# Kernel optimization log

Hardware: AMD Instinct MI355X
Metric: run time of the kernel (lower is better)

Reference implementation:

```python
import jax, jax.numpy as jnp
import numpy as np

N, E, H = 4096, 32768, 4
NUM_GRAPHS = 8
NEG_SLOPE_ATT = 0.2   # GATConv internal leaky_relu
NEG_SLOPE_ACT = 0.01  # F.leaky_relu default


def _glorot(k, shape):
    lim = (6.0 / (shape[0] + shape[-1])) ** 0.5
    return jax.random.uniform(k, shape, jnp.float32, -lim, lim)


def setup_inputs() -> dict:
    key = jax.random.key(0)
    ks = jax.random.split(key, 24)
    d = {}
    d["x_graph"] = jax.random.normal(ks[0], (N, 256), jnp.float32)
    d["action"] = jax.random.normal(ks[1], (N, 128), jnp.float32)
    d["temp_img"] = jax.random.normal(ks[2], (N, 128), jnp.float32)
    d["edge_attr"] = jax.random.normal(ks[3], (E, 16), jnp.float32)
    d["edge_index"] = jax.random.randint(ks[4], (2, E), 0, N)
    d["batch"] = jnp.sort(jax.random.randint(ks[5], (N,), 0, NUM_GRAPHS))
    # conv1: GATConv(512 -> 512, heads=4, edge_dim=16)
    d["W1"] = _glorot(ks[6], (512, H * 512))
    d["att_src1"] = _glorot(ks[7], (H, 512))
    d["att_dst1"] = _glorot(ks[8], (H, 512))
    d["att_edge1"] = _glorot(ks[9], (H, 512))
    d["We1"] = _glorot(ks[10], (16, H * 512))
    d["b1"] = jnp.zeros((H * 512,), jnp.float32)
    # conv2: GATConv(2048 -> 2048, heads=4, edge_dim=16)
    d["W2"] = _glorot(ks[11], (2048, H * 2048))
    d["att_src2"] = _glorot(ks[12], (H, 2048))
    d["att_dst2"] = _glorot(ks[13], (H, 2048))
    d["att_edge2"] = _glorot(ks[14], (H, 2048))
    d["We2"] = _glorot(ks[15], (16, H * 2048))
    d["b2"] = jnp.zeros((H * 2048,), jnp.float32)
    # fc_output: Linear(512*heads*heads=8192 -> 256)
    d["Wout"] = _glorot(ks[16], (8192, 256))
    d["bout"] = jnp.zeros((256,), jnp.float32)
    return d


def _gat(x, src, dst, eattr, W, a_s, a_d, a_e, We, b, C):
    # PyG GATConv: shared lin for src/dst, edge features in attention, softmax per dst.
    h = (x @ W).reshape(N, H, C)             # [N,H,C]
    ea = (eattr @ We).reshape(-1, H, C)      # [Ef,H,C]
    e = (h * a_s).sum(-1)[src] + (h * a_d).sum(-1)[dst] + (ea * a_e).sum(-1)  # [Ef,H]
    e = jax.nn.leaky_relu(e, NEG_SLOPE_ATT)
    m = jax.ops.segment_max(e, dst, num_segments=N)      # self-loops ensure every dst occupied
    ex = jnp.exp(e - m[dst])
    s = jax.ops.segment_sum(ex, dst, num_segments=N)
    alpha = ex / s[dst]                                   # [Ef,H]
    out = jax.ops.segment_sum(alpha[:, :, None] * h[src], dst, num_segments=N)  # [N,H,C]
    return out.reshape(N, H * C) + b


def _forward(x_graph, action, temp_img, edge_attr,
             W1, att_src1, att_dst1, att_edge1, We1, b1,
             W2, att_src2, att_dst2, att_edge2, We2, b2,
             Wout, bout, edge_index, batch):
    x = jnp.concatenate([x_graph, action, temp_img], axis=1)  # [N,512]
    src, dst = edge_index[0], edge_index[1]
    # add self-loops with fill_value='mean' for edge_attr (mean of incoming edge attrs)
    deg = jax.ops.segment_sum(jnp.ones((E,), x.dtype), dst, num_segments=N)
    loop_attr = jax.ops.segment_sum(edge_attr, dst, num_segments=N) / jnp.maximum(deg, 1.0)[:, None]
    loop = jnp.arange(N)
    src_f = jnp.concatenate([src, loop])
    dst_f = jnp.concatenate([dst, loop])
    ea_f = jnp.concatenate([edge_attr, loop_attr], axis=0)
    x = jax.nn.leaky_relu(_gat(x, src_f, dst_f, ea_f, W1, att_src1, att_dst1, att_edge1, We1, b1, 512), NEG_SLOPE_ACT)
    x = jax.nn.leaky_relu(_gat(x, src_f, dst_f, ea_f, W2, att_src2, att_dst2, att_edge2, We2, b2, 2048), NEG_SLOPE_ACT)
    x = jax.nn.leaky_relu(x @ Wout + bout, NEG_SLOPE_ACT)     # [N,256]
    sums = jax.ops.segment_sum(x, batch, num_segments=NUM_GRAPHS)
    cnt = jax.ops.segment_sum(jnp.ones((N,), x.dtype), batch, num_segments=NUM_GRAPHS)
    return sums / jnp.maximum(cnt, 1.0)[:, None]              # [NUM_GRAPHS,256]


def reference(x_graph, action, temp_img, edge_attr,
              W1, att_src1, att_dst1, att_edge1, We1, b1,
              W2, att_src2, att_dst2, att_edge2, We2, b2,
              Wout, bout, edge_index, batch):
    return _forward(x_graph, action, temp_img, edge_attr,
                    W1, att_src1, att_dst1, att_edge1, We1, b1,
                    W2, att_src2, att_dst2, att_edge2, We2, b2,
                    Wout, bout, edge_index, batch)
```

## Files before the change

kernel.cpp:

```cpp
#include <hip/hip_runtime.h>
#include <math.h>

constexpr int Nn  = 4096;
constexpr int Ne  = 32768;
constexpr int NEf = Ne + Nn;

constexpr size_t OFF_X    = 0;
constexpr size_t OFF_WT1H = 0;
constexpr size_t OFF_WT1L = 524288;
constexpr size_t OFF_Z1HI = 2097152;
constexpr size_t OFF_Z1LO = 6291456;
constexpr size_t OFF_X2HI = 2097152;
constexpr size_t OFF_X2LO = 6291456;
constexpr size_t OFF_PART = 2097152;
constexpr size_t OFF_X2   = 10485760;
constexpr size_t OFF_X3   = 10485760;
constexpr size_t OFF_H    = 18874368;
constexpr size_t OFF_WOH  = 25165824;
constexpr size_t OFF_WOL  = 26214400;
constexpr size_t OFF_YP   = 27262976;
constexpr size_t OFF_LP  = 31457280;
constexpr size_t OFF_WS1 = OFF_LP  + 65536;
constexpr size_t OFF_WD1 = OFF_WS1 + 2048;
constexpr size_t OFF_WS2 = OFF_WD1 + 2048;
constexpr size_t OFF_WD2 = OFF_WS2 + 8192;
constexpr size_t OFF_AE1 = OFF_WD2 + 8192;
constexpr size_t OFF_AE2 = OFF_AE1 + 64;
constexpr size_t OFF_AS1 = OFF_AE2 + 64;
constexpr size_t OFF_AD1 = OFF_AS1 + 16384;
constexpr size_t OFF_AS2 = OFF_AD1 + 16384;
constexpr size_t OFF_AD2 = OFF_AS2 + 16384;
constexpr size_t OFF_EB  = OFF_AD2 + 16384;
constexpr size_t OFF_AL  = OFF_EB  + (size_t)NEf*4;
constexpr size_t OFF_I   = OFF_AL  + (size_t)NEf*4;
constexpr size_t I_DEG = 0;
constexpr size_t I_RP  = 4096;
constexpr size_t I_CUR = 8200;
constexpr size_t I_EID = 12296;
constexpr size_t WS_FLOATS = OFF_I + I_EID + (size_t)NEf + 64;

using bf16x8 = __bf16 __attribute__((ext_vector_type(8)));
using f16x8  = _Float16 __attribute__((ext_vector_type(8)));
using f32x4  = float __attribute__((ext_vector_type(4)));

__device__ __forceinline__ float wred64(float v){
#pragma unroll
  for (int o = 32; o > 0; o >>= 1) v += __shfl_down(v, o, 64);
  return v;
}
__device__ __forceinline__ float lrelu(float v, float s){ return v > 0.f ? v : s * v; }

__device__ __forceinline__ unsigned short f2bf(float x){
  unsigned int u = __float_as_uint(x);
  unsigned int r = (u + 0x7FFFu + ((u >> 16) & 1u)) >> 16;
  return (unsigned short)r;
}
__device__ __forceinline__ float bf2f(unsigned short h){
  return __uint_as_float((unsigned int)h << 16);
}
__device__ __forceinline__ void split2(float x, unsigned short& h, unsigned short& l){
  h = f2bf(x);
  l = f2bf(x - bf2f(h));
}
__device__ __forceinline__ unsigned short f2h(float x){
  _Float16 h = (_Float16)x;
  return __builtin_bit_cast(unsigned short, h);
}
__device__ __forceinline__ float h2f(unsigned short u){
  return (float)__builtin_bit_cast(_Float16, u);
}
__device__ __forceinline__ void split2h(float x, unsigned short& h, unsigned short& l){
  _Float16 hh = (_Float16)x;
  h = __builtin_bit_cast(unsigned short, hh);
  _Float16 ll = (_Float16)(x - (float)hh);
  l = __builtin_bit_cast(unsigned short, ll);
}
__device__ __forceinline__ void gload16(const void* g, void* l){
  __builtin_amdgcn_global_load_lds((const __attribute__((address_space(1))) void*)g,
                                   (__attribute__((address_space(3))) void*)l, 16, 0, 0);
}

__global__ void k_concat(const float* __restrict__ xg, const float* __restrict__ ac,
                         const float* __restrict__ ti, float* __restrict__ x){
  int i = blockIdx.x * 256 + threadIdx.x;
  int n = i >> 9, c = i & 511;
  float v;
  if (c < 256)      v = xg[(size_t)n*256 + c];
  else if (c < 384) v = ac[(size_t)n*128 + (c-256)];
  else              v = ti[(size_t)n*128 + (c-384)];
  x[i] = v;
}

__global__ void k_count(const int* __restrict__ ei, int* __restrict__ deg){
  int e = blockIdx.x * 256 + threadIdx.x;
  if (e < Ne) atomicAdd(&deg[ei[Ne + e]], 1);
}

__global__ void k_scan(const int* __restrict__ deg, int* __restrict__ rowptr, int* __restrict__ cursor){
  __shared__ int sd[1024];
  int t = threadIdx.x;
  int v[4]; int s = 0;
#pragma unroll
  for (int i = 0; i < 4; i++){ v[i] = s; s += deg[t*4 + i] + 1; }
  sd[t] = s;
  __syncthreads();
  for (int off = 1; off < 1024; off <<= 1){
    int x = (t >= off) ? sd[t - off] : 0;
    __syncthreads();
    sd[t] += x;
    __syncthreads();
  }
  int base = (t == 0) ? 0 : sd[t - 1];
#pragma unroll
  for (int i = 0; i < 4; i++){ int rp = base + v[i]; rowptr[t*4 + i] = rp; cursor[t*4 + i] = rp; }
  if (t == 1023) rowptr[4096] = sd[1023];
}

__global__ void k_fill(const int* __restrict__ ei, int* __restrict__ cursor, int* __restrict__ eids){
  int e = blockIdx.x * 256 + threadIdx.x;
  if (e >= NEf) return;
  int d = (e < Ne) ? ei[Ne + e] : (e - Ne);
  int p = atomicAdd(&cursor[d], 1);
  eids[p] = e;
}

__global__ void k_sort(const int* __restrict__ rowptr, int* __restrict__ eids){
  int n = blockIdx.x * 256 + threadIdx.x;
  if (n >= Nn) return;
  int b = rowptr[n], e = rowptr[n + 1];
  for (int i = b + 1; i < e; i++){
    int key = eids[i]; int j = i - 1;
    while (j >= b && eids[j] > key){ eids[j+1] = eids[j]; j--; }
    eids[j+1] = key;
  }
}

__global__ void k_loopattr(const float* __restrict__ eattr, const int* __restrict__ rowptr,
                           const int* __restrict__ eids, float* __restrict__ lp){
  int idx = blockIdx.x * 256 + threadIdx.x;
  int n = idx >> 4, a = idx & 15;
  if (n >= Nn) return;
  int b = rowptr[n], e = rowptr[n + 1];
  float s = 0.f; int cnt = 0;
  for (int j = b; j < e; ++j){
    int id = eids[j];
    if (id < Ne){ s += eattr[(size_t)id*16 + a]; cnt++; }
  }
  lp[(size_t)n*16 + a] = s / fmaxf((float)cnt, 1.f);
}

__global__ void k_proj(const float* __restrict__ W, const float* __restrict__ a_s,
                       const float* __restrict__ a_d, float* __restrict__ Ws,
                       float* __restrict__ Wd, int K, int C){
  int gid = blockIdx.x * 256 + threadIdx.x;
  int wave = gid >> 6, lane = gid & 63;
  int h = wave & 3, k = wave >> 2;
  if (k >= K) return;
  const float* wrow = W + (size_t)k * (4*C) + (size_t)h * C;
  const float* ar = a_s + (size_t)h * C;
  const float* dr = a_d + (size_t)h * C;
  float ps = 0.f, pd = 0.f;
  for (int c = lane; c < C; c += 64){ float w = wrow[c]; ps += w * ar[c]; pd += w * dr[c]; }
  ps = wred64(ps); pd = wred64(pd);
  if (lane == 0){ Ws[k*4 + h] = ps; Wd[k*4 + h] = pd; }
}

__global__ void k_aeproj(const float* __restrict__ We, const float* __restrict__ ae,
                         float* __restrict__ outp, int C){
  int gid = blockIdx.x * 256 + threadIdx.x;
  int wave = gid >> 6, lane = gid & 63;
  int h = wave & 3, k = wave >> 2;
  if (k >= 16) return;
  const float* wrow = We + (size_t)k * (4*C) + (size_t)h * C;
  const float* ar = ae + (size_t)h * C;
  float s = 0.f;
  for (int c = lane; c < C; c += 64) s += wrow[c] * ar[c];
  s = wred64(s);
  if (lane == 0) outp[k*4 + h] = s;
}

__global__ __launch_bounds__(256) void k_asad(const float* __restrict__ x, const float* __restrict__ Ws,
                      const float* __restrict__ Wd, float* __restrict__ as_,
                      float* __restrict__ ad_, int D){
  int n = blockIdx.x, t = threadIdx.x;
  const float* row = x + (size_t)n * D;
  float p[8] = {0,0,0,0,0,0,0,0};
  for (int c = t; c < D; c += 256){
    float xv = row[c];
    float4 ws4 = *(const float4*)&Ws[c*4];
    float4 wd4 = *(const float4*)&Wd[c*4];
    p[0] += xv * ws4.x; p[1] += xv * ws4.y; p[2] += xv * ws4.z; p[3] += xv * ws4.w;
    p[4] += xv * wd4.x; p[5] += xv * wd4.y; p[6] += xv * wd4.z; p[7] += xv * wd4.w;
  }
  __shared__ float sm[4][8];
  int lane = t & 63, wid = t >> 6;
#pragma unroll
  for (int q = 0; q < 8; q++){
    float v = wred64(p[q]);
    if (lane == 0) sm[wid][q] = v;
  }
  __syncthreads();
  if (t < 8){
    float s = sm[0][t] + sm[1][t] + sm[2][t] + sm[3][t];
    if (t < 4) as_[(size_t)n*4 + t] = s;
    else       ad_[(size_t)n*4 + (t-4)] = s;
  }
}

__global__ void k_edge(const float* __restrict__ eattr, const float* __restrict__ lp,
                       const int* __restrict__ ei, const float* __restrict__ as_,
                       const float* __restrict__ ad_, const float* __restrict__ aep,
                       float* __restrict__ ebuf){
  int e = blockIdx.x * 256 + threadIdx.x;
  if (e >= NEf) return;
  int s, d; const float* ea;
  if (e < Ne){ s = ei[e]; d = ei[Ne + e]; ea = eattr + (size_t)e * 16; }
  else { s = e - Ne; d = e - Ne; ea = lp + (size_t)(e - Ne) * 16; }
  float eav[16];
#pragma unroll
  for (int k = 0; k < 16; k++) eav[k] = ea[k];
#pragma unroll
  for (int h = 0; h < 4; h++){
    float v = as_[(size_t)s*4 + h] + ad_[(size_t)d*4 + h];
#pragma unroll
    for (int k = 0; k < 16; k++) v += eav[k] * aep[k*4 + h];
    ebuf[(size_t)e*4 + h] = lrelu(v, 0.2f);
  }
}

__global__ __launch_bounds__(256) void k_softmax(const int* __restrict__ rowptr, const int* __restrict__ eids,
                          const float* __restrict__ ebuf, float* __restrict__ alpha){
  const int wid = threadIdx.x >> 6, lane = threadIdx.x & 63;
  const int n = blockIdx.x * 4 + wid;
  const int b = rowptr[n], e = rowptr[n + 1];
  float4 m = {-1e30f, -1e30f, -1e30f, -1e30f};
  for (int j = b + lane; j < e; j += 64){
    float4 ev = *(const float4*)&ebuf[(size_t)eids[j]*4];
    m.x = fmaxf(m.x, ev.x); m.y = fmaxf(m.y, ev.y);
    m.z = fmaxf(m.z, ev.z); m.w = fmaxf(m.w, ev.w);
  }
#pragma unroll
  for (int o = 32; o > 0; o >>= 1){
    m.x = fmaxf(m.x, __shfl_xor(m.x, o, 64));
    m.y = fmaxf(m.y, __shfl_xor(m.y, o, 64));
    m.z = fmaxf(m.z, __shfl_xor(m.z, o, 64));
    m.w = fmaxf(m.w, __shfl_xor(m.w, o, 64));
  }
  float4 s = {0.f, 0.f, 0.f, 0.f};
  for (int j = b + lane; j < e; j += 64){
    int eid = eids[j];
    float4 ev = *(const float4*)&ebuf[(size_t)eid*4];
    float4 ex = { expf(ev.x - m.x), expf(ev.y - m.y), expf(ev.z - m.z), expf(ev.w - m.w) };
    *(float4*)&alpha[(size_t)eid*4] = ex;
    s.x += ex.x; s.y += ex.y; s.z += ex.z; s.w += ex.w;
  }
#pragma unroll
  for (int o = 32; o > 0; o >>= 1){
    s.x += __shfl_xor(s.x, o, 64);
    s.y += __shfl_xor(s.y, o, 64);
    s.z += __shfl_xor(s.z, o, 64);
    s.w += __shfl_xor(s.w, o, 64);
  }
  float4 r = { 1.f/s.x, 1.f/s.y, 1.f/s.z, 1.f/s.w };
  for (int j = b + lane; j < e; j += 64){
    int eid = eids[j];
    float4 av = *(const float4*)&alpha[(size_t)eid*4];
    av.x *= r.x; av.y *= r.y; av.z *= r.z; av.w *= r.w;
    *(float4*)&alpha[(size_t)eid*4] = av;
  }
}

__global__ __launch_bounds__(256) void k_agg1_split(const float* __restrict__ x, const float* __restrict__ alpha,
                      const int* __restrict__ rowptr, const int* __restrict__ eids,
                      const int* __restrict__ ei, unsigned short* __restrict__ z1hi,
                      unsigned short* __restrict__ z1lo){
  int n = blockIdx.x, t = threadIdx.x;
  float2 a0 = {0,0}, a1 = {0,0}, a2 = {0,0}, a3 = {0,0};
  int b = rowptr[n], e = rowptr[n + 1];
  for (int j = b; j < e; ++j){
    int eid = eids[j];
    int s = (eid < Ne) ? ei[eid] : (eid - Ne);
    float4 av = *(const float4*)&alpha[(size_t)eid*4];
    float2 xv = *(const float2*)&x[(size_t)s*512 + t*2];
    a0.x += av.x*xv.x; a0.y += av.x*xv.y;
    a1.x += av.y*xv.x; a1.y += av.y*xv.y;
    a2.x += av.z*xv.x; a2.y += av.z*xv.y;
    a3.x += av.w*xv.x; a3.y += av.w*xv.y;
  }
  size_t base = (size_t)n*2048 + t*2;
  float2 av[4] = {a0, a1, a2, a3};
#pragma unroll
  for (int h = 0; h < 4; h++){
    ushort2 hh, ll;
    split2(av[h].x, hh.x, ll.x);
    split2(av[h].y, hh.y, ll.y);
    *(ushort2*)&z1hi[base + h*512] = hh;
    *(ushort2*)&z1lo[base + h*512] = ll;
  }
}

__global__ void k_splitx2(const float* __restrict__ x2, unsigned short* __restrict__ xh,
                          unsigned short* __restrict__ xl){
  int i = blockIdx.x * 256 + threadIdx.x;
  float4 v = ((const float4*)x2)[i];
  ushort4 h, l;
  split2h(v.x, h.x, l.x); split2h(v.y, h.y, l.y);
  split2h(v.z, h.z, l.z); split2h(v.w, h.w, l.w);
  ((ushort4*)xh)[i] = h;
  ((ushort4*)xl)[i] = l;
}

__global__ __launch_bounds__(256) void k_agg2b(const unsigned short* __restrict__ H,
                      const float* __restrict__ alpha,
                      const int* __restrict__ rowptr, const int* __restrict__ eids,
                      const int* __restrict__ ei, unsigned short* __restrict__ x3,
                      const float* __restrict__ b2, int h){
  int n = blockIdx.x, t = threadIdx.x;
  float acc[8] = {0,0,0,0,0,0,0,0};
  int b = rowptr[n], e = rowptr[n + 1];
  for (int j = b; j < e; ++j){
    int eid = eids[j];
    int s = (eid < Ne) ? ei[eid] : (eid - Ne);
    float a = alpha[(size_t)eid*4 + h];
    f16x8 hv = *(const f16x8*)&H[(size_t)s*2048 + t*8];
#pragma unroll
    for (int q = 0; q < 8; q++) acc[q] += a * (float)hv[q];
  }
  const float* bb = b2 + (size_t)h*2048 + t*8;
  ushort4 o0, o1;
  float4 b0 = *(const float4*)bb;
  float4 b1 = *(const float4*)(bb + 4);
  o0.x = f2h(lrelu(acc[0] + b0.x, 0.01f)); o0.y = f2h(lrelu(acc[1] + b0.y, 0.01f));
  o0.z = f2h(lrelu(acc[2] + b0.z, 0.01f)); o0.w = f2h(lrelu(acc[3] + b0.w, 0.01f));
  o1.x = f2h(lrelu(acc[4] + b1.x, 0.01f)); o1.y = f2h(lrelu(acc[5] + b1.y, 0.01f));
  o1.z = f2h(lrelu(acc[6] + b1.z, 0.01f)); o1.w = f2h(lrelu(acc[7] + b1.w, 0.01f));
  size_t base = (size_t)n*2048 + t*8;
  *(ushort4*)&x3[base]     = o0;
  *(ushort4*)&x3[base + 4] = o1;
}

template<bool HALF, bool STORELO>
__global__ __launch_bounds__(256) void k_wsplit(const float* __restrict__ W, int ldw, int coloff, int K,
                       unsigned short* __restrict__ whi, unsigned short* __restrict__ wlo){
  __shared__ float tile[32][33];
  int bk = blockIdx.x * 32, bn = blockIdx.y * 32;
  int tx = threadIdx.x & 31, ty = threadIdx.x >> 5;
#pragma unroll
  for (int i = 0; i < 4; i++){
    int k = bk + ty + i*8;
    tile[ty + i*8][tx] = W[(size_t)k*ldw + coloff + bn + tx];
  }
  __syncthreads();
#pragma unroll
  for (int i = 0; i < 4; i++){
    int n = bn + ty + i*8;
    float v = tile[tx][ty + i*8];
    unsigned short hh, ll;
    if (HALF) split2h(v, hh, ll); else split2(v, hh, ll);
    whi[(size_t)n*K + bk + tx] = hh;
    if (STORELO) wlo[(size_t)n*K + bk + tx] = ll;
  }
}

__global__ __launch_bounds__(512) void k_gemm256(
    const unsigned short* __restrict__ Ah, const unsigned short* __restrict__ Al,
    const unsigned short* __restrict__ Bh, unsigned short* __restrict__ Cout)
{
  __shared__ __align__(16) unsigned short lds[49152];
  const int t = threadIdx.x;
  const int bid = blockIdx.y * 8 + blockIdx.x;
  const int sbid = (bid & 7) * 32 + (bid >> 3);
  const int brow = (sbid >> 3) * 128, bcol = (sbid & 7) * 256;
  const int w = t >> 6, lane = t & 63;
  const int wm = (w >> 2) * 64, wn = (w & 3) * 64;
  constexpr int BUF = 16384, BOFF = 8192;

  const int asr = t >> 3;
  const int ascc = (t & 7) ^ (asr & 7);
  const unsigned short* asrc = (ascc < 4 ? Ah : Al) + (size_t)(brow + asr)*2048 + (size_t)(ascc & 3)*8;
  const int bsr = t >> 2;
  const int bscc = (t & 3) ^ ((bsr >> 1) & 3);
  const unsigned short* bsrc = Bh + (size_t)(bcol + bsr)*2048 + (size_t)bscc*8;
  const int adst = w * 512;
  const int bdst = BOFF + w * 512;

  const int fr = lane & 15, kc = lane >> 4;
  const int aswz = (kc ^ (lane & 7)) * 8;
  const int bswz = (kc ^ ((lane >> 1) & 3)) * 8;
  int aoff[4], boff[4];
#pragma unroll
  for (int m = 0; m < 4; m++) aoff[m] = (wm + m*16 + fr)*64 + aswz;
#pragma unroll
  for (int n = 0; n < 4; n++) boff[n] = BOFF + (wn + n*16 + fr)*32 + bswz;

  f32x4 acc[4][4];
#pragma unroll
  for (int m = 0; m < 4; m++)
#pragma unroll
    for (int n = 0; n < 4; n++) acc[m][n] = f32x4{0.f, 0.f, 0.f, 0.f};

  gload16(asrc,                        &lds[adst]);
  gload16(asrc + (size_t)64*2048,      &lds[4096 + adst]);
  gload16(bsrc,                        &lds[bdst]);
  gload16(bsrc + (size_t)128*2048,     &lds[4096 + bdst]);
  gload16(asrc + 32,                   &lds[BUF + adst]);
  gload16(asrc + (size_t)64*2048 + 32, &lds[BUF + 4096 + adst]);
  gload16(bsrc + 32,                   &lds[BUF + bdst]);
  gload16(bsrc + (size_t)128*2048 + 32,&lds[BUF + 4096 + bdst]);
  asm volatile("s_waitcnt vmcnt(4)" ::: "memory");
  __builtin_amdgcn_s_barrier();

  for (int kt = 0; kt < 64; ++kt){
    const int bufo = (kt % 3) * BUF;
    const int nbo  = ((kt + 2) % 3) * BUF;
    const size_t nko = (size_t)(kt + 2) * 32;
    const bool pf = (kt + 2) < 64;

    f16x8 ah[4], al[4];
#pragma unroll
    for (int m = 0; m < 4; m++){
      ah[m] = *(const f16x8*)&lds[bufo + aoff[m]];
      al[m] = *(const f16x8*)&lds[bufo + (aoff[m] ^ 32)];
    }
    {
      f16x8 b0 = *(const f16x8*)&lds[bufo + boff[0]];
      f16x8 b1 = *(const f16x8*)&lds[bufo + boff[1]];
      if (pf){
        gload16(asrc + nko,                   &lds[nbo + adst]);
        gload16(asrc + (size_t)64*2048 + nko, &lds[nbo + 4096 + adst]);
      }
      __builtin_amdgcn_s_barrier();
      asm volatile("s_waitcnt lgkmcnt(0)");
      __builtin_amdgcn_s_setprio(1);
#pragma unroll
      for (int m = 0; m < 4; m++) acc[m][0] = __builtin_amdgcn_mfma_f32_16x16x32_f16(ah[m], b0, acc[m][0], 0, 0, 0);
#pragma unroll
      for (int m = 0; m < 4; m++) acc[m][0] = __builtin_amdgcn_mfma_f32_16x16x32_f16(al[m], b0, acc[m][0], 0, 0, 0);
#pragma unroll
      for (int m = 0; m < 4; m++) acc[m][1] = __builtin_amdgcn_mfma_f32_16x16x32_f16(ah[m], b1, acc[m][1], 0, 0, 0);
#pragma unroll
      for (int m = 0; m < 4; m++) acc[m][1] = __builtin_amdgcn_mfma_f32_16x16x32_f16(al[m], b1, acc[m][1], 0, 0, 0);
      __builtin_amdgcn_s_setprio(0);
      __builtin_amdgcn_s_barrier();
    }
    {
      f16x8 b2 = *(const f16x8*)&lds[bufo + boff[2]];
      f16x8 b3 = *(const f16x8*)&lds[bufo + boff[3]];
      if (pf){
        gload16(bsrc + nko,                    &lds[nbo + bdst]);
        gload16(bsrc + (size_t)128*2048 + nko, &lds[nbo + 4096 + bdst]);
      }
      __builtin_amdgcn_s_barrier();
      asm volatile("s_waitcnt lgkmcnt(0)");
      __builtin_amdgcn_s_setprio(1);
#pragma unroll
      for (int m = 0; m < 4; m++) acc[m][2] = __builtin_amdgcn_mfma_f32_16x16x32_f16(ah[m], b2, acc[m][2], 0, 0, 0);
#pragma unroll
      for (int m = 0; m < 4; m++) acc[m][2] = __builtin_amdgcn_mfma_f32_16x16x32_f16(al[m], b2, acc[m][2], 0, 0, 0);
#pragma unroll
      for (int m = 0; m < 4; m++) acc[m][3] = __builtin_amdgcn_mfma_f32_16x16x32_f16(ah[m], b3, acc[m][3], 0, 0, 0);
#pragma unroll
      for (int m = 0; m < 4; m++) acc[m][3] = __builtin_amdgcn_mfma_f32_16x16x32_f16(al[m], b3, acc[m][3], 0, 0, 0);
      __builtin_amdgcn_s_setprio(0);
      __builtin_amdgcn_s_barrier();
    }
    if (pf) asm volatile("s_waitcnt vmcnt(4)" ::: "memory");
    else    asm volatile("s_waitcnt vmcnt(0)" ::: "memory");
    __builtin_amdgcn_s_barrier();
  }

#pragma unroll
  for (int m = 0; m < 4; m++){
    const int row0 = brow + wm + m*16 + kc*4;
#pragma unroll
    for (int n = 0; n < 4; n++){
      const int col = bcol + wn + n*16 + fr;
#pragma unroll
      for (int r = 0; r < 4; r++)
        Cout[(size_t)(row0 + r)*2048 + col] = f2h(acc[m][n][r]);
    }
  }
}

template<int KLEN, bool EXACTA, bool HALF, bool OUTF32, bool BETA1, bool ACT, bool HASBIAS>
__global__ __launch_bounds__(256) void k_gemm2(
    const unsigned short* __restrict__ Ah, const unsigned short* __restrict__ Al, int lda, size_t az,
    const unsigned short* __restrict__ Bh, const unsigned short* __restrict__ Bl, int ldb, size_t bz,
    void* __restrict__ Cout, int ldc, size_t cz,
    const float* __restrict__ bias, size_t biasz)
{
  __shared__ unsigned short lds[16384];
  const int t = threadIdx.x;
  const int z = blockIdx.z;
  const int brow = blockIdx.y * 128, bcol = blockIdx.x * 128;
  const int wid = t >> 6, lane = t & 63;
  const int wm = (wid >> 1) * 64, wn = (wid & 1) * 64;

  const int sr = t >> 3, sc = t & 7;
  const int scc = sc ^ (sr & 7);
  const unsigned short* asrc = (scc < 4 ? Ah : Al) + (size_t)(brow + sr)*lda + (size_t)z*az + (size_t)(scc & 3)*8;
  const unsigned short* bsrc = (scc < 4 ? Bh : Bl) + (size_t)(bcol + sr)*ldb + (size_t)z*bz + (size_t)(scc & 3)*8;
  unsigned short* adst = &lds[(size_t)wid * 512];
  unsigned short* bdst = &lds[8192 + (size_t)wid * 512];

  const int fr = lane & 15, kc = lane >> 4;
  const int swz = ((kc ^ (lane & 7)) << 3);
  int aoff[4], boff[4];
#pragma unroll
  for (int m = 0; m < 4; m++) aoff[m] = (wm + m*16 + fr)*64 + swz;
#pragma unroll
  for (int n = 0; n < 4; n++) boff[n] = 8192 + (wn + n*16 + fr)*64 + swz;

  f32x4 acc[4][4];
#pragma unroll
  for (int m = 0; m < 4; m++)
#pragma unroll
    for (int n = 0; n < 4; n++) acc[m][n] = f32x4{0.f, 0.f, 0.f, 0.f};

  for (int kt = 0; kt < KLEN/32; ++kt){
    const size_t ko = (size_t)kt * 32;
#pragma unroll
    for (int i = 0; i < 4; i++){
      gload16(asrc + (size_t)i*32*lda + ko, adst + i*2048);
      gload16(bsrc + (size_t)i*32*ldb + ko, bdst + i*2048);
    }
    __syncthreads();

    if (HALF){
      f16x8 ah[4], bh[4], bl[4];
#pragma unroll
      for (int m = 0; m < 4; m++) ah[m] = *(const f16x8*)&lds[aoff[m]];
#pragma unroll
      for (int n = 0; n < 4; n++){
        bh[n] = *(const f16x8*)&lds[boff[n]];
        bl[n] = *(const f16x8*)&lds[boff[n] ^ 32];
      }
#pragma unroll
      for (int m = 0; m < 4; m++)
#pragma unroll
        for (int n = 0; n < 4; n++){
          acc[m][n] = __builtin_amdgcn_mfma_f32_16x16x32_f16(ah[m], bh[n], acc[m][n], 0, 0, 0);
          acc[m][n] = __builtin_amdgcn_mfma_f32_16x16x32_f16(ah[m], bl[n], acc[m][n], 0, 0, 0);
        }
    } else {
      bf16x8 ah[4], al[4], bh[4], bl[4];
#pragma unroll
      for (int m = 0; m < 4; m++){
        ah[m] = *(const bf16x8*)&lds[aoff[m]];
        if (!EXACTA) al[m] = *(const bf16x8*)&lds[aoff[m] ^ 32];
      }
#pragma unroll
      for (int n = 0; n < 4; n++){
        bh[n] = *(const bf16x8*)&lds[boff[n]];
        bl[n] = *(const bf16x8*)&lds[boff[n] ^ 32];
      }
#pragma unroll
      for (int m = 0; m < 4; m++)
#pragma unroll
        for (int n = 0; n < 4; n++){
          acc[m][n] = __builtin_amdgcn_mfma_f32_16x16x32_bf16(ah[m], bh[n], acc[m][n], 0, 0, 0);
          acc[m][n] = __builtin_amdgcn_mfma_f32_16x16x32_bf16(ah[m], bl[n], acc[m][n], 0, 0, 0);
          if (!EXACTA)
            acc[m][n] = __builtin_amdgcn_mfma_f32_16x16x32_bf16(al[m], bh[n], acc[m][n], 0, 0, 0);
        }
    }
    __syncthreads();
  }

  float bv[4] = {0.f, 0.f, 0.f, 0.f};
  if (HASBIAS){
#pragma unroll
    for (int n = 0; n < 4; n++) bv[n] = bias[(size_t)z*biasz + bcol + wn + n*16 + fr];
  }
  float* Cf = (float*)Cout + (size_t)z*cz;
  unsigned short* Cb = (unsigned short*)Cout + (size_t)z*cz;
#pragma unroll
  for (int m = 0; m < 4; m++){
    const int row0 = brow + wm + m*16 + kc*4;
#pragma unroll
    for (int n = 0; n < 4; n++){
      const int col = bcol + wn + n*16 + fr;
#pragma unroll
      for (int r = 0; r < 4; r++){
        float v = acc[m][n][r] + bv[n];
        if (ACT) v = lrelu(v, 0.01f);
        if (OUTF32){
          float* cp = &Cf[(size_t)(row0 + r)*ldc + col];
          if (BETA1) v += *cp;
          *cp = v;
        } else {
          Cb[(size_t)(row0 + r)*ldc + col] = f2bf(v);
        }
      }
    }
  }
}

__global__ void k_gsum(const float* __restrict__ yp, const float* __restrict__ bout,
                       const int* __restrict__ batch, float* __restrict__ part){
  const int s = blockIdx.x, g = blockIdx.y, t = threadIdx.x;
  __shared__ int sb[2];
  if (t < 2){
    int key = g + t, lo = 0, hi = Nn;
    while (lo < hi){ int mid = (lo + hi) >> 1; if (batch[mid] < key) lo = mid + 1; else hi = mid; }
    sb[t] = lo;
  }
  __syncthreads();
  const int b = sb[0], e = sb[1];
  const size_t P = (size_t)Nn * 256;
  float acc = 0.f;
  float bt = bout[t];
  for (int n = b + s; n < e; n += 32){
    size_t i = (size_t)n*256 + t;
    float v = yp[i] + yp[P + i] + yp[2*P + i] + yp[3*P + i] + bt;
    acc += lrelu(v, 0.01f);
  }
  part[(size_t)(g*32 + s)*256 + t] = acc;
}

__global__ void k_gfin(const float* __restrict__ part, const int* __restrict__ batch,
                       float* __restrict__ out){
  const int g = blockIdx.x, t = threadIdx.x;
  __shared__ int sb[2];
  if (t < 2){
    int key = g + t, lo = 0, hi = Nn;
    while (lo < hi){ int mid = (lo + hi) >> 1; if (batch[mid] < key) lo = mid + 1; else hi = mid; }
    sb[t] = lo;
  }
  __syncthreads();
  const int cnt = sb[1] - sb[0];
  float s = 0.f;
#pragma unroll
  for (int k = 0; k < 32; k++) s += part[(size_t)(g*32 + k)*256 + t];
  out[g*256 + t] = s / fmaxf((float)cnt, 1.f);
}

extern "C" void kernel_launch(void* const* d_in, const int* in_sizes, int n_in,
                              void* d_out, int out_size, void* d_ws, size_t ws_size,
                              hipStream_t stream){
  const float* xg    = (const float*)d_in[0];
  const float* ac    = (const float*)d_in[1];
  const float* ti    = (const float*)d_in[2];
  const float* eattr = (const float*)d_in[3];
  const int*   ei    = (const int*)  d_in[4];
  const int*   batch = (const int*)  d_in[5];
  const float* W1    = (const float*)d_in[6];
  const float* as1w  = (const float*)d_in[7];
  const float* ad1w  = (const float*)d_in[8];
  const float* ae1w  = (const float*)d_in[9];
  const float* We1   = (const float*)d_in[10];
  const float* b1    = (const float*)d_in[11];
  const float* W2    = (const float*)d_in[12];
  const float* as2w  = (const float*)d_in[13];
  const float* ad2w  = (const float*)d_in[14];
  const float* ae2w  = (const float*)d_in[15];
  const float* We2   = (const float*)d_in[16];
  const float* b2    = (const float*)d_in[17];
  const float* Wout  = (const float*)d_in[18];
  const float* bout  = (const float*)d_in[19];
  float* out = (float*)d_out;
  float* ws  = (float*)d_ws;
  if (ws_size < WS_FLOATS * sizeof(float)) return;
  int* iws = (int*)(ws + OFF_I);

  unsigned short* z1hi = (unsigned short*)(ws + OFF_Z1HI);
  unsigned short* z1lo = (unsigned short*)(ws + OFF_Z1LO);
  unsigned short* wt1h = (unsigned short*)(ws + OFF_WT1H);
  unsigned short* wt1l = (unsigned short*)(ws + OFF_WT1L);
  unsigned short* x2hi = (unsigned short*)(ws + OFF_X2HI);
  unsigned short* x2lo = (unsigned short*)(ws + OFF_X2LO);
  unsigned short* whi  = (unsigned short*)(ws + OFF_X);
  unsigned short* woh  = (unsigned short*)(ws + OFF_WOH);
  unsigned short* wol  = (unsigned short*)(ws + OFF_WOL);
  unsigned short* Hb   = (unsigned short*)(ws + OFF_H);
  unsigned short* x3   = (unsigned short*)(ws + OFF_X3);

  hipMemsetAsync(iws + I_DEG, 0, Nn * sizeof(int), stream);
  k_concat <<<8192, 256, 0, stream>>>(xg, ac, ti, ws + OFF_X);
  k_count  <<<128,  256, 0, stream>>>(ei, iws + I_DEG);
  k_scan   <<<1,   1024, 0, stream>>>(iws + I_DEG, iws + I_RP, iws + I_CUR);
  k_fill   <<<144,  256, 0, stream>>>(ei, iws + I_CUR, iws + I_EID);
  k_sort   <<<16,   256, 0, stream>>>(iws + I_RP, iws + I_EID);
  k_loopattr<<<256, 256, 0, stream>>>(eattr, iws + I_RP, iws + I_EID, ws + OFF_LP);

  k_proj   <<<512,  256, 0, stream>>>(W1, as1w, ad1w, ws + OFF_WS1, ws + OFF_WD1, 512, 512);
  k_proj   <<<2048, 256, 0, stream>>>(W2, as2w, ad2w, ws + OFF_WS2, ws + OFF_WD2, 2048, 2048);
  k_aeproj <<<16,   256, 0, stream>>>(We1, ae1w, ws + OFF_AE1, 512);
  k_aeproj <<<16,   256, 0, stream>>>(We2, ae2w, ws + OFF_AE2, 2048);
  k_wsplit<true, true><<<dim3(256, 8), 256, 0, stream>>>(Wout, 256, 0, 8192, woh, wol);

  k_asad      <<<4096, 256, 0, stream>>>(ws + OFF_X, ws + OFF_WS1, ws + OFF_WD1, ws + OFF_AS1, ws + OFF_AD1, 512);
  k_edge      <<<144,  256, 0, stream>>>(eattr, ws + OFF_LP, ei, ws + OFF_AS1, ws + OFF_AD1, ws + OFF_AE1, ws + OFF_EB);
  k_softmax   <<<1024, 256, 0, stream>>>(iws + I_RP, iws + I_EID, ws + OFF_EB, ws + OFF_AL);
  k_agg1_split<<<4096, 256, 0, stream>>>(ws + OFF_X, ws + OFF_AL, iws + I_RP, iws + I_EID, ei, z1hi, z1lo);
  k_wsplit<false, true><<<dim3(16, 64), 256, 0, stream>>>(W1, 2048, 0, 512, wt1h, wt1l);
  k_gemm2<512, false, false, true, false, true, true><<<dim3(4, 32, 4), 256, 0, stream>>>(
      z1hi, z1lo, 2048, 512,  wt1h, wt1l, 512, 512*512,
      ws + OFF_X2, 2048, 512,  b1, 512);

  k_asad   <<<4096, 256, 0, stream>>>(ws + OFF_X2, ws + OFF_WS2, ws + OFF_WD2, ws + OFF_AS2, ws + OFF_AD2, 2048);
  k_edge   <<<144,  256, 0, stream>>>(eattr, ws + OFF_LP, ei, ws + OFF_AS2, ws + OFF_AD2, ws + OFF_AE2, ws + OFF_EB);
  k_softmax<<<1024, 256, 0, stream>>>(iws + I_RP, iws + I_EID, ws + OFF_EB, ws + OFF_AL);

  k_splitx2<<<8192, 256, 0, stream>>>(ws + OFF_X2, x2hi, x2lo);

  for (int h = 0; h < 4; ++h){
    k_wsplit<true, false><<<dim3(64, 64), 256, 0, stream>>>(W2, 8192, h*2048, 2048, whi, nullptr);
    k_gemm256 <<<dim3(8, 32), 512, 0, stream>>>(x2hi, x2lo, whi, Hb);
    k_agg2b   <<<4096, 256, 0, stream>>>(Hb, ws + OFF_AL, iws + I_RP, iws + I_EID, ei, x3, b2, h);
    if (h == 0)
      k_gemm2<512, true, true, true, false, false, false><<<dim3(2, 32, 4), 256, 0, stream>>>(
          x3, x3, 2048, 512,  woh + (size_t)h*2048, wol + (size_t)h*2048, 8192, 512,
          ws + OFF_YP, 256, (size_t)Nn*256,  nullptr, 0);
    else
      k_gemm2<512, true, true, true, true, false, false><<<dim3(2, 32, 4), 256, 0, stream>>>(
          x3, x3, 2048, 512,  woh + (size_t)h*2048, wol + (size_t)h*2048, 8192, 512,
          ws + OFF_YP, 256, (size_t)Nn*256,  nullptr, 0);
  }

  k_gsum<<<dim3(32, 8), 256, 0, stream>>>(ws + OFF_YP, bout, batch, ws + OFF_PART);
  k_gfin<<<8, 256, 0, stream>>>(ws + OFF_PART, batch, out);
}
```

Before: 735.5 us.

## Shrink gemm256 block tile to 128x128 with four waves and simpler pipeline

Changes the split-precision fp16 MFMA GEMM from a 128x256 tile with 8 waves to a 128x128 tile with 4 waves. This doubles the grid to 512 blocks and cuts LDS use so more blocks fit per CU. The main loop is also simplified: the two half-steps with their intra-iteration barriers are merged into one MFMA phase, and all prefetch loads are issued up front. The aim is better occupancy and less barrier overhead, at the cost of more global traffic per output from the smaller tile.

```diff
diff --git a/kernel.cpp b/kernel.cpp
--- a/kernel.cpp
+++ b/kernel.cpp
@@ -362,18 +362,18 @@
   }
 }
 
-__global__ __launch_bounds__(512) void k_gemm256(
+__global__ __launch_bounds__(256) void k_gemm256(
     const unsigned short* __restrict__ Ah, const unsigned short* __restrict__ Al,
     const unsigned short* __restrict__ Bh, unsigned short* __restrict__ Cout)
 {
-  __shared__ __align__(16) unsigned short lds[49152];
+  __shared__ __align__(16) unsigned short lds[36864];
   const int t = threadIdx.x;
-  const int bid = blockIdx.y * 8 + blockIdx.x;
-  const int sbid = (bid & 7) * 32 + (bid >> 3);
-  const int brow = (sbid >> 3) * 128, bcol = (sbid & 7) * 256;
+  const int bid = blockIdx.y * 16 + blockIdx.x;
+  const int sbid = (bid & 7) * 64 + (bid >> 3);
+  const int brow = (sbid >> 4) * 128, bcol = (sbid & 15) * 128;
   const int w = t >> 6, lane = t & 63;
-  const int wm = (w >> 2) * 64, wn = (w & 3) * 64;
-  constexpr int BUF = 16384, BOFF = 8192;
+  const int wm = (w >> 1) * 64, wn = (w & 1) * 64;
+  constexpr int BUF = 12288, BOFF = 8192;
 
   const int asr = t >> 3;
   const int ascc = (t & 7) ^ (asr & 7);
@@ -399,15 +399,16 @@
 #pragma unroll
     for (int n = 0; n < 4; n++) acc[m][n] = f32x4{0.f, 0.f, 0.f, 0.f};
 
-  gload16(asrc,                        &lds[adst]);
-  gload16(asrc + (size_t)64*2048,      &lds[4096 + adst]);
-  gload16(bsrc,                        &lds[bdst]);
-  gload16(bsrc + (size_t)128*2048,     &lds[4096 + bdst]);
-  gload16(asrc + 32,                   &lds[BUF + adst]);
-  gload16(asrc + (size_t)64*2048 + 32, &lds[BUF + 4096 + adst]);
-  gload16(bsrc + 32,                   &lds[BUF + bdst]);
-  gload16(bsrc + (size_t)128*2048 + 32,&lds[BUF + 4096 + bdst]);
-  asm volatile("s_waitcnt vmcnt(4)" ::: "memory");
+#pragma unroll
+  for (int tile = 0; tile < 2; tile++){
+    const int bb = tile * BUF;
+    const size_t ko = (size_t)tile * 32;
+#pragma unroll
+    for (int i = 0; i < 4; i++) gload16(asrc + (size_t)i*32*2048 + ko, &lds[bb + i*2048 + adst]);
+#pragma unroll
+    for (int i = 0; i < 2; i++) gload16(bsrc + (size_t)i*64*2048 + ko, &lds[bb + i*2048 + bdst]);
+  }
+  asm volatile("s_waitcnt vmcnt(6)" ::: "memory");
   __builtin_amdgcn_s_barrier();
 
   for (int kt = 0; kt < 64; ++kt){
@@ -416,55 +417,33 @@
     const size_t nko = (size_t)(kt + 2) * 32;
     const bool pf = (kt + 2) < 64;
 
-    f16x8 ah[4], al[4];
+    f16x8 ah[4], al[4], bfr[4];
 #pragma unroll
     for (int m = 0; m < 4; m++){
       ah[m] = *(const f16x8*)&lds[bufo + aoff[m]];
       al[m] = *(const f16x8*)&lds[bufo + (aoff[m] ^ 32)];
     }
-    {
-      f16x8 b0 = *(const f16x8*)&lds[bufo + boff[0]];
-      f16x8 b1 = *(const f16x8*)&lds[bufo + boff[1]];
-      if (pf){
-        gload16(asrc + nko,                   &lds[nbo + adst]);
-        gload16(asrc + (size_t)64*2048 + nko, &lds[nbo + 4096 + adst]);
-      }
-      __builtin_amdgcn_s_barrier();
-      asm volatile("s_waitcnt lgkmcnt(0)");
-      __builtin_amdgcn_s_setprio(1);
-#pragma unroll
-      for (int m = 0; m < 4; m++) acc[m][0] = __builtin_amdgcn_mfma_f32_16x16x32_f16(ah[m], b0, acc[m][0], 0, 0, 0);
-#pragma unroll
-      for (int m = 0; m < 4; m++) acc[m][0] = __builtin_amdgcn_mfma_f32_16x16x32_f16(al[m], b0, acc[m][0], 0, 0, 0);
-#pragma unroll
-      for (int m = 0; m < 4; m++) acc[m][1] = __builtin_amdgcn_mfma_f32_16x16x32_f16(ah[m], b1, acc[m][1], 0, 0, 0);
-#pragma unroll
-      for (int m = 0; m < 4; m++) acc[m][1] = __builtin_amdgcn_mfma_f32_16x16x32_f16(al[m], b1, acc[m][1], 0, 0, 0);
-      __builtin_amdgcn_s_setprio(0);
-      __builtin_amdgcn_s_barrier();
+#pragma unroll
+    for (int n = 0; n < 4; n++) bfr[n] = *(const f16x8*)&lds[bufo + boff[n]];
+
+    if (pf){
+#pragma unroll
+      for (int i = 0; i < 4; i++) gload16(asrc + (size_t)i*32*2048 + nko, &lds[nbo + i*2048 + adst]);
+#pragma unroll
+      for (int i = 0; i < 2; i++) gload16(bsrc + (size_t)i*64*2048 + nko, &lds[nbo + i*2048 + bdst]);
     }
-    {
-      f16x8 b2 = *(const f16x8*)&lds[bufo + boff[2]];
-      f16x8 b3 = *(const f16x8*)&lds[bufo + boff[3]];
-      if (pf){
-        gload16(bsrc + nko,                    &lds[nbo + bdst]);
-        gload16(bsrc + (size_t)128*2048 + nko, &lds[nbo + 4096 + bdst]);
-      }
-      __builtin_amdgcn_s_barrier();
-      asm volatile("s_waitcnt lgkmcnt(0)");
-      __builtin_amdgcn_s_setprio(1);
-#pragma unroll
-      for (int m = 0; m < 4; m++) acc[m][2] = __builtin_amdgcn_mfma_f32_16x16x32_f16(ah[m], b2, acc[m][2], 0, 0, 0);
-#pragma unroll
-      for (int m = 0; m < 4; m++) acc[m][2] = __builtin_amdgcn_mfma_f32_16x16x32_f16(al[m], b2, acc[m][2], 0, 0, 0);
-#pragma unroll
-      for (int m = 0; m < 4; m++) acc[m][3] = __builtin_amdgcn_mfma_f32_16x16x32_f16(ah[m], b3, acc[m][3], 0, 0, 0);
-#pragma unroll
-      for (int m = 0; m < 4; m++) acc[m][3] = __builtin_amdgcn_mfma_f32_16x16x32_f16(al[m], b3, acc[m][3], 0, 0, 0);
-      __builtin_amdgcn_s_setprio(0);
-      __builtin_amdgcn_s_barrier();
+
+    __builtin_amdgcn_s_setprio(1);
+#pragma unroll
+    for (int n = 0; n < 4; n++){
+#pragma unroll
+      for (int m = 0; m < 4; m++) acc[m][n] = __builtin_amdgcn_mfma_f32_16x16x32_f16(ah[m], bfr[n], acc[m][n], 0, 0, 0);
+#pragma unroll
+      for (int m = 0; m < 4; m++) acc[m][n] = __builtin_amdgcn_mfma_f32_16x16x32_f16(al[m], bfr[n], acc[m][n], 0, 0, 0);
     }
-    if (pf) asm volatile("s_waitcnt vmcnt(4)" ::: "memory");
+    __builtin_amdgcn_s_setprio(0);
+
+    if (pf) asm volatile("s_waitcnt vmcnt(6)" ::: "memory");
     else    asm volatile("s_waitcnt vmcnt(0)" ::: "memory");
     __builtin_amdgcn_s_barrier();
   }
@@ -706,7 +685,7 @@
 
   for (int h = 0; h < 4; ++h){
     k_wsplit<true, false><<<dim3(64, 64), 256, 0, stream>>>(W2, 8192, h*2048, 2048, whi, nullptr);
-    k_gemm256 <<<dim3(8, 32), 512, 0, stream>>>(x2hi, x2lo, whi, Hb);
+    k_gemm256 <<<dim3(16, 32), 256, 0, stream>>>(x2hi, x2lo, whi, Hb);
     k_agg2b   <<<4096, 256, 0, stream>>>(Hb, ws + OFF_AL, iws + I_RP, iws + I_EID, ei, x3, b2, h);
     if (h == 0)
       k_gemm2<512, true, true, true, false, false, false><<<dim3(2, 32, 4), 256, 0, stream>>>(
```

Result: slower. 764.8 us (+4.0%).
